# Optimization experiments

Measured on AMD Instinct MI355X. Metric: run time of the kernel, lower is better.

The kernel has to match this reference:

```python
import jax, jax.numpy as jnp
import numpy as np

N_NODES = 50000
N_EDGES = 500000
D_NODE = 64
D_EDGE = 32
MSG_DIM = 2 * D_NODE + D_EDGE      # 160
HID_DIM = MSG_DIM + D_NODE         # 224
ALPHA = 0.01                       # LeakyReLU slope


def setup_inputs() -> dict:
    key = jax.random.key(0)
    ks = jax.random.split(key, 8)
    h_n = jax.random.normal(ks[0], (N_NODES, D_NODE), dtype=jnp.float32)
    h_e = jax.random.normal(ks[1], (N_EDGES, D_EDGE), dtype=jnp.float32)
    src = jax.random.randint(ks[2], (N_EDGES,), 0, N_NODES, dtype=jnp.int32)
    dst = jax.random.randint(ks[3], (N_EDGES,), 0, N_NODES, dtype=jnp.int32)
    W_msg = jax.random.normal(ks[4], (MSG_DIM, MSG_DIM), dtype=jnp.float32) * 0.05
    b_msg = jax.random.normal(ks[5], (MSG_DIM,), dtype=jnp.float32) * 0.05
    W_hid = jax.random.normal(ks[6], (HID_DIM, HID_DIM), dtype=jnp.float32) * 0.05
    b_hid = jax.random.normal(ks[7], (HID_DIM,), dtype=jnp.float32) * 0.05
    return {"h_n": h_n, "h_e": h_e, "src": src, "dst": dst,
            "W_msg": W_msg, "b_msg": b_msg, "W_hid": W_hid, "b_hid": b_hid}


def reference(h_n, h_e, src, dst, W_msg, b_msg, W_hid, b_hid):
    # --- message: gather src/dst node features + edge features, linear + leaky_relu ---
    m_input = jnp.concatenate([h_n[src], h_n[dst], h_e], axis=-1)   # [E, MSG_DIM]
    m = jax.nn.leaky_relu(m_input @ W_msg.T + b_msg, negative_slope=ALPHA)
    # --- reduce: sum messages at destination nodes (DGL fn.sum) ---
    m_sum = jax.ops.segment_sum(m, dst, num_segments=N_NODES)       # [N, MSG_DIM]
    # --- update: concat(m_sum, h_n), linear + leaky_relu ---
    h_input = jnp.concatenate([m_sum, h_n], axis=-1)                # [N, HID_DIM]
    h_out = jax.nn.leaky_relu(h_input @ W_hid.T + b_hid, negative_slope=ALPHA)
    # single graph with unique node ids: split/squeeze is identity
    return h_out
```

## Files before the change

### kernel.cpp

```cpp
#include <hip/hip_runtime.h>

#define N_NODES 50000
#define N_EDGES 500000
#define D_NODE 64
#define D_EDGE 32
#define MSG_DIM 160
#define HID_DIM 224
#define ALPHA 0.01f

#define FNB 16
#define NBKT 3125
#define BKT_CAP 256
#define A_STRIDE 168
#define MT_STRIDE 72
#define CURSOR_PAD 16
#define CVT_BLKS 3200
#define SCAT_BLKS 1954

typedef unsigned short u16;
typedef unsigned long long u64;
typedef short short8 __attribute__((ext_vector_type(8)));
typedef float float4v __attribute__((ext_vector_type(4)));

static __device__ __forceinline__ u16 f2bf(float f) {
    unsigned int u = __float_as_uint(f);
    u += 0x7fffu + ((u >> 16) & 1u);
    return (u16)(u >> 16);
}

__global__ __launch_bounds__(256) void cvt_scatter(const float* __restrict__ h_n,
                                                   const float* __restrict__ W_msg,
                                                   const float* __restrict__ W_hid,
                                                   const int* __restrict__ src,
                                                   const int* __restrict__ dst,
                                                   u16* __restrict__ hn_bf,
                                                   u16* __restrict__ Wm_bf,
                                                   u16* __restrict__ Wh_bf,
                                                   int* __restrict__ cursor,
                                                   u64* __restrict__ pack) {
    const int b = blockIdx.x;
    if (b < CVT_BLKS) {
        int i = b * 256 + threadIdx.x;
        const float* in; u16* outp; int j;
        if (i < 800000)      { in = h_n;   outp = hn_bf; j = i; }
        else if (i < 806400) { in = W_msg; outp = Wm_bf; j = i - 800000; }
        else if (i < 818944) { in = W_hid; outp = Wh_bf; j = i - 806400; }
        else return;
        float4 v = reinterpret_cast<const float4*>(in)[j];
        ushort4 o;
        o.x = f2bf(v.x); o.y = f2bf(v.y); o.z = f2bf(v.z); o.w = f2bf(v.w);
        reinterpret_cast<ushort4*>(outp)[j] = o;
    } else {
        int e = (b - CVT_BLKS) * 256 + threadIdx.x;
        if (e < N_EDGES) {
            int d = dst[e];
            int bk = d >> 4;
            int idx = atomicAdd(&cursor[bk * CURSOR_PAD], 1);
            if (idx < BKT_CAP)
                pack[(size_t)bk * BKT_CAP + idx] =
                    ((u64)e << 34) | ((u64)d << 17) | (u64)src[e];
        }
    }
}

__global__ __launch_bounds__(256) void fused_kernel(
    const u16* __restrict__ hn_bf, const float* __restrict__ h_e,
    const u64* __restrict__ pack, const int* __restrict__ cursor,
    const u16* __restrict__ Wm_bf, const float* __restrict__ b_msg,
    const u16* __restrict__ Wh_bf, const float* __restrict__ b_hid,
    float* __restrict__ out)
{
    __shared__ alignas(16) u16 X_lds[64 * A_STRIDE];
    __shared__ alignas(16) u16 MT[4 * 16 * MT_STRIDE];
    __shared__ alignas(16) u16 dst16[64];

    const int tid = threadIdx.x;
    const int n0 = blockIdx.x * FNB;
    const int p_begin = blockIdx.x * BKT_CAP;
    int ecnt = cursor[blockIdx.x * CURSOR_PAD];
    if (ecnt > BKT_CAP) ecnt = BKT_CAP;
    const int p_end = p_begin + ecnt;

    const int wave = tid >> 6, lane = tid & 63;
    const int qd = lane >> 4, l15 = lane & 15;
    const int e_loc = tid >> 2, j4 = tid & 3;

    const int nchunk = (wave < 2) ? 3 : 2;
    float biasv[3];
#pragma unroll
    for (int ci = 0; ci < 3; ++ci) {
        const int c = wave + ci * 4;
        biasv[ci] = (c < 10) ? b_msg[c * 16 + l15] : 0.f;
    }
    float4v m_acc[3] = {{0,0,0,0},{0,0,0,0},{0,0,0,0}};
    u16* MTw = &MT[wave * 16 * MT_STRIDE];

    u64 pk_cur = 0, pk_nxt = 0;
    uint4 sA, sB, dA, dB;
    float4 heA, heB;
    if (p_begin < p_end) {
        int pp = p_begin + e_loc;
        int pidx = (pp < p_end) ? pp : (p_end - 1);
        pk_cur = pack[pidx];
        const int s  = (int)(pk_cur & 0x1FFFF);
        const int d  = (int)((pk_cur >> 17) & 0x1FFFF);
        const int eo = (int)(pk_cur >> 34);
        const uint4* srow = reinterpret_cast<const uint4*>(hn_bf + (size_t)s * D_NODE);
        const uint4* drow = reinterpret_cast<const uint4*>(hn_bf + (size_t)d * D_NODE);
        sA = srow[j4 * 2]; sB = srow[j4 * 2 + 1];
        dA = drow[j4 * 2]; dB = drow[j4 * 2 + 1];
        const float4* he = reinterpret_cast<const float4*>(h_e + (size_t)eo * D_EDGE);
        heA = he[j4 * 2]; heB = he[j4 * 2 + 1];
        int pp1 = pp + 64;
        pk_nxt = pack[(pp1 < p_end) ? pp1 : (p_end - 1)];
    }

    for (int p0 = p_begin; p0 < p_end; p0 += 64) {
        {
            const bool padE = (p0 + e_loc >= p_end);
            const int d = (int)((pk_cur >> 17) & 0x1FFFF);
            if (j4 == 0) dst16[e_loc] = padE ? (u16)0xFFFFu : (u16)(d - n0);
            uint4* Arow = reinterpret_cast<uint4*>(&X_lds[e_loc * A_STRIDE]);
            Arow[j4 * 2]     = sA;
            Arow[j4 * 2 + 1] = sB;
            Arow[8 + j4 * 2]     = dA;
            Arow[8 + j4 * 2 + 1] = dB;
            ushort4 lo, hi;
            lo.x = f2bf(heA.x); lo.y = f2bf(heA.y); lo.z = f2bf(heA.z); lo.w = f2bf(heA.w);
            hi.x = f2bf(heB.x); hi.y = f2bf(heB.y); hi.z = f2bf(heB.z); hi.w = f2bf(heB.w);
            ushort4* Aus = reinterpret_cast<ushort4*>(Arow);
            Aus[32 + j4 * 2]     = lo;
            Aus[32 + j4 * 2 + 1] = hi;
        }
        __syncthreads();

        short8 xf[4][5];
#pragma unroll
        for (int s = 0; s < 4; ++s)
#pragma unroll
            for (int ks = 0; ks < 5; ++ks)
                xf[s][ks] = *reinterpret_cast<const short8*>(
                    &X_lds[(s * 16 + l15) * A_STRIDE + ks * 32 + qd * 8]);

        short8 a2[2];
#pragma unroll
        for (int fi = 0; fi < 2; ++fi) {
            short8 dv = *reinterpret_cast<const short8*>(&dst16[fi * 32 + qd * 8]);
            short8 t;
#pragma unroll
            for (int j = 0; j < 8; ++j)
                t[j] = (short)(((int)(u16)dv[j] == l15) ? 0x3F80 : 0);
            a2[fi] = t;
        }

        if (p0 + 64 < p_end) {
            pk_cur = pk_nxt;
            const int s  = (int)(pk_cur & 0x1FFFF);
            const int eo = (int)(pk_cur >> 34);
            const int d  = (int)((pk_cur >> 17) & 0x1FFFF);
            const uint4* srow = reinterpret_cast<const uint4*>(hn_bf + (size_t)s * D_NODE);
            const uint4* drow = reinterpret_cast<const uint4*>(hn_bf + (size_t)d * D_NODE);
            sA = srow[j4 * 2]; sB = srow[j4 * 2 + 1];
            dA = drow[j4 * 2]; dB = drow[j4 * 2 + 1];
            const float4* he = reinterpret_cast<const float4*>(h_e + (size_t)eo * D_EDGE);
            heA = he[j4 * 2]; heB = he[j4 * 2 + 1];
            int pp2 = p0 + 128 + e_loc;
            pk_nxt = pack[(pp2 < p_end) ? pp2 : (p_end - 1)];
        }
        __syncthreads();

        for (int ci = 0; ci < nchunk; ++ci) {
            const int c = wave + ci * 4;
            const int fbase = c * 16;
            short8 wf[5];
#pragma unroll
            for (int ks = 0; ks < 5; ++ks)
                wf[ks] = *reinterpret_cast<const short8*>(
                    Wm_bf + (size_t)(fbase + l15) * MSG_DIM + ks * 32 + qd * 8);
            const float bias = biasv[ci];
#pragma unroll
            for (int s = 0; s < 4; ++s) {
                float4v acc = {0.f, 0.f, 0.f, 0.f};
#pragma unroll
                for (int ks = 0; ks < 5; ++ks)
                    acc = __builtin_amdgcn_mfma_f32_16x16x32_bf16(xf[s][ks], wf[ks], acc, 0, 0, 0);
                float v0 = acc[0] + bias, v1 = acc[1] + bias,
                      v2 = acc[2] + bias, v3 = acc[3] + bias;
                v0 = fmaxf(v0, ALPHA * v0); v1 = fmaxf(v1, ALPHA * v1);
                v2 = fmaxf(v2, ALPHA * v2); v3 = fmaxf(v3, ALPHA * v3);
                ushort4 m4;
                m4.x = f2bf(v0); m4.y = f2bf(v1); m4.z = f2bf(v2); m4.w = f2bf(v3);
                *reinterpret_cast<ushort4*>(&MTw[l15 * MT_STRIDE + s * 16 + qd * 4]) = m4;
            }
            short8 b2_0 = *reinterpret_cast<const short8*>(&MTw[l15 * MT_STRIDE + qd * 8]);
            short8 b2_1 = *reinterpret_cast<const short8*>(&MTw[l15 * MT_STRIDE + 32 + qd * 8]);
            m_acc[ci] = __builtin_amdgcn_mfma_f32_16x16x32_bf16(a2[0], b2_0, m_acc[ci], 0, 0, 0);
            m_acc[ci] = __builtin_amdgcn_mfma_f32_16x16x32_bf16(a2[1], b2_1, m_acc[ci], 0, 0, 0);
        }
    }
    __syncthreads();

    u16* Xb = X_lds;
    for (int ci = 0; ci < nchunk; ++ci) {
        const int c = wave + ci * 4;
#pragma unroll
        for (int r = 0; r < 4; ++r)
            Xb[(qd * 4 + r) * A_STRIDE + c * 16 + l15] = f2bf(m_acc[ci][r]);
    }
    __syncthreads();

    const int node = n0 + l15;
    short8 b_frag[7];
#pragma unroll
    for (int ks = 0; ks < 5; ++ks)
        b_frag[ks] = *reinterpret_cast<const short8*>(
            &Xb[l15 * A_STRIDE + ks * 32 + qd * 8]);
#pragma unroll
    for (int ks = 5; ks < 7; ++ks)
        b_frag[ks] = *reinterpret_cast<const short8*>(
            hn_bf + (size_t)node * D_NODE + (ks - 5) * 32 + qd * 8);

    for (int c = wave; c < 14; c += 4) {
        float4v acc = {0.f, 0.f, 0.f, 0.f};
#pragma unroll
        for (int ks = 0; ks < 7; ++ks) {
            short8 a = *reinterpret_cast<const short8*>(
                Wh_bf + (size_t)(c * 16 + l15) * HID_DIM + ks * 32 + qd * 8);
            acc = __builtin_amdgcn_mfma_f32_16x16x32_bf16(a, b_frag[ks], acc, 0, 0, 0);
        }
        const float4 bias = *reinterpret_cast<const float4*>(b_hid + c * 16 + qd * 4);
        float v0 = acc[0] + bias.x, v1 = acc[1] + bias.y,
              v2 = acc[2] + bias.z, v3 = acc[3] + bias.w;
        v0 = fmaxf(v0, ALPHA * v0); v1 = fmaxf(v1, ALPHA * v1);
        v2 = fmaxf(v2, ALPHA * v2); v3 = fmaxf(v3, ALPHA * v3);
        float4 o; o.x = v0; o.y = v1; o.z = v2; o.w = v3;
        *reinterpret_cast<float4*>(&out[(size_t)node * HID_DIM + c * 16 + qd * 4]) = o;
    }
}

extern "C" void kernel_launch(void* const* d_in, const int* in_sizes, int n_in,
                              void* d_out, int out_size, void* d_ws, size_t ws_size,
                              hipStream_t stream)
{
    const float* h_n   = (const float*)d_in[0];
    const float* h_e   = (const float*)d_in[1];
    const int*   src   = (const int*)d_in[2];
    const int*   dst   = (const int*)d_in[3];
    const float* W_msg = (const float*)d_in[4];
    const float* b_msg = (const float*)d_in[5];
    const float* W_hid = (const float*)d_in[6];
    const float* b_hid = (const float*)d_in[7];
    float* out = (float*)d_out;

    char* ws = (char*)d_ws;
    u16* hn_bf  = (u16*)(ws + 0);
    u16* Wm_bf  = (u16*)(ws + 6400000);
    u16* Wh_bf  = (u16*)(ws + 6451200);
    int* cursor = (int*)(ws + 6551552);
    u64* pack   = (u64*)(ws + 6751552);

    hipMemsetAsync(cursor, 0, (size_t)NBKT * CURSOR_PAD * sizeof(int), stream);
    cvt_scatter<<<CVT_BLKS + SCAT_BLKS, 256, 0, stream>>>(
        h_n, W_msg, W_hid, src, dst, hn_bf, Wm_bf, Wh_bf, cursor, pack);
    fused_kernel<<<NBKT, 256, 0, stream>>>(
        hn_bf, h_e, pack, cursor, Wm_bf, b_msg, Wh_bf, b_hid, out);
}
```

Before: 271.8 us.

## Replace LDS message transpose with cross-lane shuffles and drop register prefetch

```diff
diff --git a/kernel.cpp b/kernel.cpp
--- a/kernel.cpp
+++ b/kernel.cpp
@@ -12,7 +12,6 @@
 #define NBKT 3125
 #define BKT_CAP 256
 #define A_STRIDE 168
-#define MT_STRIDE 72
 #define CURSOR_PAD 16
 #define CVT_BLKS 3200
 #define SCAT_BLKS 1954
@@ -71,7 +70,6 @@
     float* __restrict__ out)
 {
     __shared__ alignas(16) u16 X_lds[64 * A_STRIDE];
-    __shared__ alignas(16) u16 MT[4 * 16 * MT_STRIDE];
     __shared__ alignas(16) u16 dst16[64];
 
     const int tid = threadIdx.x;
@@ -85,6 +83,10 @@
     const int qd = lane >> 4, l15 = lane & 15;
     const int e_loc = tid >> 2, j4 = tid & 3;
 
+    const int srcA = ((qd & 1) * 2) * 16 + l15;
+    const int srcB = srcA + 16;
+    const bool hi2 = (qd >> 1) != 0;
+
     const int nchunk = (wave < 2) ? 3 : 2;
     float biasv[3];
 #pragma unroll
@@ -93,41 +95,28 @@
         biasv[ci] = (c < 10) ? b_msg[c * 16 + l15] : 0.f;
     }
     float4v m_acc[3] = {{0,0,0,0},{0,0,0,0},{0,0,0,0}};
-    u16* MTw = &MT[wave * 16 * MT_STRIDE];
-
-    u64 pk_cur = 0, pk_nxt = 0;
-    uint4 sA, sB, dA, dB;
-    float4 heA, heB;
-    if (p_begin < p_end) {
-        int pp = p_begin + e_loc;
-        int pidx = (pp < p_end) ? pp : (p_end - 1);
-        pk_cur = pack[pidx];
-        const int s  = (int)(pk_cur & 0x1FFFF);
-        const int d  = (int)((pk_cur >> 17) & 0x1FFFF);
-        const int eo = (int)(pk_cur >> 34);
-        const uint4* srow = reinterpret_cast<const uint4*>(hn_bf + (size_t)s * D_NODE);
-        const uint4* drow = reinterpret_cast<const uint4*>(hn_bf + (size_t)d * D_NODE);
-        sA = srow[j4 * 2]; sB = srow[j4 * 2 + 1];
-        dA = drow[j4 * 2]; dB = drow[j4 * 2 + 1];
-        const float4* he = reinterpret_cast<const float4*>(h_e + (size_t)eo * D_EDGE);
-        heA = he[j4 * 2]; heB = he[j4 * 2 + 1];
-        int pp1 = pp + 64;
-        pk_nxt = pack[(pp1 < p_end) ? pp1 : (p_end - 1)];
-    }
 
     for (int p0 = p_begin; p0 < p_end; p0 += 64) {
         {
-            const bool padE = (p0 + e_loc >= p_end);
-            const int d = (int)((pk_cur >> 17) & 0x1FFFF);
+            int pp = p0 + e_loc;
+            const bool padE = (pp >= p_end); if (padE) pp = p_end - 1;
+            const u64 pk = pack[pp];
+            const int s  = (int)(pk & 0x1FFFF);
+            const int d  = (int)((pk >> 17) & 0x1FFFF);
+            const int eo = (int)(pk >> 34);
             if (j4 == 0) dst16[e_loc] = padE ? (u16)0xFFFFu : (u16)(d - n0);
+            const uint4* srow = reinterpret_cast<const uint4*>(hn_bf + (size_t)s * D_NODE);
+            const uint4* drow = reinterpret_cast<const uint4*>(hn_bf + (size_t)d * D_NODE);
             uint4* Arow = reinterpret_cast<uint4*>(&X_lds[e_loc * A_STRIDE]);
-            Arow[j4 * 2]     = sA;
-            Arow[j4 * 2 + 1] = sB;
-            Arow[8 + j4 * 2]     = dA;
-            Arow[8 + j4 * 2 + 1] = dB;
+            Arow[j4 * 2]     = srow[j4 * 2];
+            Arow[j4 * 2 + 1] = srow[j4 * 2 + 1];
+            Arow[8 + j4 * 2]     = drow[j4 * 2];
+            Arow[8 + j4 * 2 + 1] = drow[j4 * 2 + 1];
+            const float4* he = reinterpret_cast<const float4*>(h_e + (size_t)eo * D_EDGE);
+            float4 p = he[j4 * 2], q = he[j4 * 2 + 1];
             ushort4 lo, hi;
-            lo.x = f2bf(heA.x); lo.y = f2bf(heA.y); lo.z = f2bf(heA.z); lo.w = f2bf(heA.w);
-            hi.x = f2bf(heB.x); hi.y = f2bf(heB.y); hi.z = f2bf(heB.z); hi.w = f2bf(heB.w);
+            lo.x = f2bf(p.x); lo.y = f2bf(p.y); lo.z = f2bf(p.z); lo.w = f2bf(p.w);
+            hi.x = f2bf(q.x); hi.y = f2bf(q.y); hi.z = f2bf(q.z); hi.w = f2bf(q.w);
             ushort4* Aus = reinterpret_cast<ushort4*>(Arow);
             Aus[32 + j4 * 2]     = lo;
             Aus[32 + j4 * 2 + 1] = hi;
@@ -151,21 +140,6 @@
             for (int j = 0; j < 8; ++j)
                 t[j] = (short)(((int)(u16)dv[j] == l15) ? 0x3F80 : 0);
             a2[fi] = t;
-        }
-
-        if (p0 + 64 < p_end) {
-            pk_cur = pk_nxt;
-            const int s  = (int)(pk_cur & 0x1FFFF);
-            const int eo = (int)(pk_cur >> 34);
-            const int d  = (int)((pk_cur >> 17) & 0x1FFFF);
-            const uint4* srow = reinterpret_cast<const uint4*>(hn_bf + (size_t)s * D_NODE);
-            const uint4* drow = reinterpret_cast<const uint4*>(hn_bf + (size_t)d * D_NODE);
-            sA = srow[j4 * 2]; sB = srow[j4 * 2 + 1];
-            dA = drow[j4 * 2]; dB = drow[j4 * 2 + 1];
-            const float4* he = reinterpret_cast<const float4*>(h_e + (size_t)eo * D_EDGE);
-            heA = he[j4 * 2]; heB = he[j4 * 2 + 1];
-            int pp2 = p0 + 128 + e_loc;
-            pk_nxt = pack[(pp2 < p_end) ? pp2 : (p_end - 1)];
         }
         __syncthreads();
 
@@ -178,6 +152,8 @@
                 wf[ks] = *reinterpret_cast<const short8*>(
                     Wm_bf + (size_t)(fbase + l15) * MSG_DIM + ks * 32 + qd * 8);
             const float bias = biasv[ci];
+            int mlo[4], mhi[4];
+            __builtin_amdgcn_s_setprio(1);
 #pragma unroll
             for (int s = 0; s < 4; ++s) {
                 float4v acc = {0.f, 0.f, 0.f, 0.f};
@@ -188,14 +164,25 @@
                       v2 = acc[2] + bias, v3 = acc[3] + bias;
                 v0 = fmaxf(v0, ALPHA * v0); v1 = fmaxf(v1, ALPHA * v1);
                 v2 = fmaxf(v2, ALPHA * v2); v3 = fmaxf(v3, ALPHA * v3);
-                ushort4 m4;
-                m4.x = f2bf(v0); m4.y = f2bf(v1); m4.z = f2bf(v2); m4.w = f2bf(v3);
-                *reinterpret_cast<ushort4*>(&MTw[l15 * MT_STRIDE + s * 16 + qd * 4]) = m4;
+                mlo[s] = (int)((unsigned)f2bf(v0) | ((unsigned)f2bf(v1) << 16));
+                mhi[s] = (int)((unsigned)f2bf(v2) | ((unsigned)f2bf(v3) << 16));
             }
-            short8 b2_0 = *reinterpret_cast<const short8*>(&MTw[l15 * MT_STRIDE + qd * 8]);
-            short8 b2_1 = *reinterpret_cast<const short8*>(&MTw[l15 * MT_STRIDE + 32 + qd * 8]);
-            m_acc[ci] = __builtin_amdgcn_mfma_f32_16x16x32_bf16(a2[0], b2_0, m_acc[ci], 0, 0, 0);
-            m_acc[ci] = __builtin_amdgcn_mfma_f32_16x16x32_bf16(a2[1], b2_1, m_acc[ci], 0, 0, 0);
+#pragma unroll
+            for (int fi = 0; fi < 2; ++fi) {
+                const int s0 = fi * 2, s1 = fi * 2 + 1;
+                int aL0 = __shfl(mlo[s0], srcA), aL1 = __shfl(mlo[s1], srcA);
+                int aH0 = __shfl(mhi[s0], srcA), aH1 = __shfl(mhi[s1], srcA);
+                int bL0 = __shfl(mlo[s0], srcB), bL1 = __shfl(mlo[s1], srcB);
+                int bH0 = __shfl(mhi[s0], srcB), bH1 = __shfl(mhi[s1], srcB);
+                uint4 t;
+                t.x = (unsigned)(hi2 ? aL1 : aL0);
+                t.y = (unsigned)(hi2 ? aH1 : aH0);
+                t.z = (unsigned)(hi2 ? bL1 : bL0);
+                t.w = (unsigned)(hi2 ? bH1 : bH0);
+                short8 b2 = *reinterpret_cast<short8*>(&t);
+                m_acc[ci] = __builtin_amdgcn_mfma_f32_16x16x32_bf16(a2[fi], b2, m_acc[ci], 0, 0, 0);
+            }
+            __builtin_amdgcn_s_setprio(0);
         }
     }
     __syncthreads();
```

After: 273.6 us. Within noise of the previous version (+0.6%).
